# Optimization experiments

Hardware: AMD Instinct MI355X
Metric: run time of the kernel (lower is better)

Reference implementation:

```python
import jax, jax.numpy as jnp
import numpy as np

N_NODES = 100000
N_EDGES = 1600000
HIDDEN = 128
STEPS = 4
N_GRAPHS = 64


def setup_inputs() -> dict:
    key = jax.random.key(0)
    ks = jax.random.split(key, 8)
    x = jax.random.normal(ks[0], (N_NODES, HIDDEN), dtype=jnp.float32)
    edge_index = jax.random.randint(ks[1], (2, N_EDGES), 0, N_NODES, dtype=jnp.int64)
    batch = jnp.sort(jax.random.randint(ks[2], (N_NODES,), 0, N_GRAPHS, dtype=jnp.int64))
    s = 1.0 / np.sqrt(HIDDEN)
    weight = jax.random.normal(ks[3], (STEPS, HIDDEN, HIDDEN), dtype=jnp.float32) * s
    w_ih = jax.random.normal(ks[4], (3 * HIDDEN, HIDDEN), dtype=jnp.float32) * s
    w_hh = jax.random.normal(ks[5], (3 * HIDDEN, HIDDEN), dtype=jnp.float32) * s
    b_ih = jnp.zeros((3 * HIDDEN,), dtype=jnp.float32)
    b_hh = jnp.zeros((3 * HIDDEN,), dtype=jnp.float32)
    return {"x": x, "edge_index": edge_index, "batch": batch,
            "weight": weight, "w_ih": w_ih, "w_hh": w_hh,
            "b_ih": b_ih, "b_hh": b_hh}


def _gru_cell(m, h, w_ih, w_hh, b_ih, b_hh):
    # PyTorch GRUCell: gates ordered (r, z, n)
    gi = m @ w_ih.T + b_ih  # [N, 3H]
    gh = h @ w_hh.T + b_hh  # [N, 3H]
    i_r, i_z, i_n = jnp.split(gi, 3, axis=-1)
    h_r, h_z, h_n = jnp.split(gh, 3, axis=-1)
    r = jax.nn.sigmoid(i_r + h_r)
    z = jax.nn.sigmoid(i_z + h_z)
    n = jnp.tanh(i_n + r * h_n)
    return (1.0 - z) * n + z * h


def reference(x, edge_index, batch, weight, w_ih, w_hh, b_ih, b_hh):
    src, dst = edge_index[0], edge_index[1]
    h = x
    for i in range(STEPS):
        m = h @ weight[i]  # [N, H]
        # message = m[src] scattered (add) into dst
        aggr = jax.ops.segment_sum(m[src], dst, num_segments=N_NODES)
        h = _gru_cell(aggr, h, w_ih, w_hh, b_ih, b_hh)
    h = jax.nn.relu(h)
    # global mean pool per graph
    sums = jax.ops.segment_sum(h, batch, num_segments=N_GRAPHS)  # [G, H]
    counts = jax.ops.segment_sum(jnp.ones((N_NODES,), h.dtype), batch, num_segments=N_GRAPHS)
    return sums / jnp.maximum(counts, 1.0)[:, None]
```

## Files before the change

kernel.cpp:

```cpp
#include <hip/hip_runtime.h>

#define N_NODES  100000
#define N_EDGES  1600000
#define HIDDEN   128
#define STEPS    4
#define N_GRAPHS 64
#define NBUCK    256
#define BWID     391
#define BCAP     7168
#define OUT_P    136

typedef unsigned short u16;
typedef unsigned int   u32;
typedef unsigned long long u64;
typedef __attribute__((ext_vector_type(8))) short bf16x8;
typedef __attribute__((ext_vector_type(4))) float f32x4;

__device__ inline u16 f2bf(float f) {
  u32 u = __float_as_uint(f);
  u = (u + 0x7FFFu + ((u >> 16) & 1u)) >> 16;
  return (u16)u;
}
__device__ inline float bf2f(u16 b) { return __uint_as_float(((u32)b) << 16); }

__device__ inline float fast_sig(float x) { return 1.f / (1.f + __expf(-x)); }
__device__ inline float fast_tanh(float x) {
  x = fminf(fmaxf(x, -15.f), 15.f);
  float e = __expf(2.f * x);
  return (e - 1.f) / (e + 1.f);
}

__global__ __launch_bounds__(1024) void k_part(const int* __restrict__ esrc,
                                               const int* __restrict__ edst,
                                               int* __restrict__ gcursor,
                                               u64* __restrict__ ebuf) {
  __shared__ int hist[NBUCK];
  __shared__ int base[NBUCK];
  int tid = threadIdx.x;
  if (tid < NBUCK) hist[tid] = 0;
  __syncthreads();
  int e0 = blockIdx.x * 4096;
  int sv[4], dv[4], bk[4], rk[4];
  #pragma unroll
  for (int i = 0; i < 4; ++i) {
    int e = e0 + i * 1024 + tid;
    if (e < N_EDGES) {
      sv[i] = esrc[e];
      dv[i] = edst[e];
      bk[i] = (int)((u32)dv[i] / (u32)BWID);
      rk[i] = atomicAdd(&hist[bk[i]], 1);
    } else bk[i] = -1;
  }
  __syncthreads();
  if (tid < NBUCK) base[tid] = atomicAdd(&gcursor[tid], hist[tid]);
  __syncthreads();
  #pragma unroll
  for (int i = 0; i < 4; ++i) {
    if (bk[i] >= 0) {
      int pos = bk[i] * BCAP + base[bk[i]] + rk[i];
      ebuf[pos] = ((u64)(u32)dv[i] << 32) | (u32)sv[i];
    }
  }
}

__global__ void k_bscan(const int* __restrict__ gcursor, int* __restrict__ ebase) {
  __shared__ int buf[NBUCK];
  int t = threadIdx.x;
  int v = gcursor[t];
  buf[t] = v;
  __syncthreads();
  for (int off = 1; off < NBUCK; off <<= 1) {
    int u = 0;
    if (t >= off) u = buf[t - off];
    __syncthreads();
    buf[t] += u;
    __syncthreads();
  }
  ebase[t] = buf[t] - v;
  if (t == NBUCK - 1) ebase[NBUCK] = buf[t];
}

__global__ __launch_bounds__(1024) void k_csr(const u64* __restrict__ ebuf,
                                              const int* __restrict__ ebase,
                                              int* __restrict__ offs,
                                              int* __restrict__ csr) {
  __shared__ int lcnt[512];
  __shared__ int lofs[512];
  int b = blockIdx.x, tid = threadIdx.x;
  int n0 = b * BWID;
  int n1 = min(n0 + BWID, N_NODES);
  int nn = n1 - n0;
  int e0 = ebase[b];
  int cnt = ebase[b + 1] - e0;
  const u64* ebase_p = ebuf + (size_t)b * BCAP;
  if (tid < 512) lcnt[tid] = 0;
  __syncthreads();
  for (int e = tid; e < cnt; e += 1024) {
    int dst = (int)(ebase_p[e] >> 32);
    atomicAdd(&lcnt[dst - n0], 1);
  }
  __syncthreads();
  if (tid < 512) lofs[tid] = lcnt[tid];
  __syncthreads();
  for (int off = 1; off < 512; off <<= 1) {
    int v = 0;
    if (tid < 512 && tid >= off) v = lofs[tid - off];
    __syncthreads();
    if (tid < 512 && tid >= off) lofs[tid] += v;
    __syncthreads();
  }
  int nodeoff = 0;
  if (tid < 512) nodeoff = e0 + lofs[tid] - lcnt[tid];
  if (tid < 512) lofs[tid] = nodeoff;
  if (tid < nn) offs[n0 + tid] = nodeoff;
  if (b == 0 && tid == 0) offs[N_NODES] = N_EDGES;
  __syncthreads();
  for (int e = tid; e < cnt; e += 1024) {
    u64 p = ebase_p[e];
    int src = (int)(p & 0xffffffffull);
    int dst = (int)(p >> 32);
    int pos = atomicAdd(&lofs[dst - n0], 1);
    csr[pos] = src;
  }
}

__global__ void k_wb(const float* __restrict__ W, const float* __restrict__ w_ih,
                     const float* __restrict__ w_hh, u16* __restrict__ bsw) {
  __shared__ float wrow[128];
  int b = blockIdx.x, st = b >> 8, k = b & 255, t = threadIdx.x;
  if (k < 128) wrow[t] = W[(st * 128 + k) * 128 + t];
  __syncthreads();
  int kc = k >> 5, quad = (k >> 3) & 3, kl = k & 7;
  u16* base = bsw + (size_t)st * 131072 + kc * 16384;
  #pragma unroll
  for (int gq = 0; gq < 4; ++gq) {
    int c = gq * 128 + t;
    float v;
    if (k < 128) {
      if (c < 384) {
        const float* wr = w_ih + c * 128;
        float sacc = 0.f;
        for (int j = 0; j < 128; ++j) sacc += wrow[j] * wr[j];
        v = sacc;
      } else v = 0.f;
    } else {
      int kk = k - 128;
      if (c < 256)      v = w_hh[c * 128 + kk];
      else if (c < 384) v = 0.f;
      else              v = w_hh[(c - 128) * 128 + kk];
    }
    int gi = c >> 7, cw = c & 127;
    int wv = cw >> 5, hu = (cw >> 4) & 1, nl = c & 15;
    int slot = wv * 8 + gi * 2 + hu;
    base[(slot * 4 + quad) * 128 + nl * 8 + kl] = f2bf(v);
  }
}

__global__ void k_convert(const float* __restrict__ x, u16* __restrict__ h) {
  int i = (blockIdx.x * 256 + threadIdx.x) * 4;
  float4 v = *(const float4*)(x + i);
  u16 o[4] = {f2bf(v.x), f2bf(v.y), f2bf(v.z), f2bf(v.w)};
  *(uint2*)(h + i) = *(uint2*)o;
}

__global__ void k_gather(const u16* __restrict__ h, const int* __restrict__ csr,
                         const int* __restrict__ offs, u16* __restrict__ s) {
  int node = blockIdx.x * 4 + (threadIdx.x >> 6);
  int lane = threadIdx.x & 63;
  int beg = offs[node], end = offs[node + 1];
  float a0 = 0.f, a1 = 0.f;
  int j = beg;
  for (; j + 8 <= end; j += 8) {
    int i0 = csr[j],     i1 = csr[j + 1], i2 = csr[j + 2], i3 = csr[j + 3];
    int i4 = csr[j + 4], i5 = csr[j + 5], i6 = csr[j + 6], i7 = csr[j + 7];
    u32 v0 = *(const u32*)(h + (size_t)i0 * 128 + lane * 2);
    u32 v1 = *(const u32*)(h + (size_t)i1 * 128 + lane * 2);
    u32 v2 = *(const u32*)(h + (size_t)i2 * 128 + lane * 2);
    u32 v3 = *(const u32*)(h + (size_t)i3 * 128 + lane * 2);
    u32 v4 = *(const u32*)(h + (size_t)i4 * 128 + lane * 2);
    u32 v5 = *(const u32*)(h + (size_t)i5 * 128 + lane * 2);
    u32 v6 = *(const u32*)(h + (size_t)i6 * 128 + lane * 2);
    u32 v7 = *(const u32*)(h + (size_t)i7 * 128 + lane * 2);
    a0 += __uint_as_float(v0 << 16); a1 += __uint_as_float(v0 & 0xffff0000u);
    a0 += __uint_as_float(v1 << 16); a1 += __uint_as_float(v1 & 0xffff0000u);
    a0 += __uint_as_float(v2 << 16); a1 += __uint_as_float(v2 & 0xffff0000u);
    a0 += __uint_as_float(v3 << 16); a1 += __uint_as_float(v3 & 0xffff0000u);
    a0 += __uint_as_float(v4 << 16); a1 += __uint_as_float(v4 & 0xffff0000u);
    a0 += __uint_as_float(v5 << 16); a1 += __uint_as_float(v5 & 0xffff0000u);
    a0 += __uint_as_float(v6 << 16); a1 += __uint_as_float(v6 & 0xffff0000u);
    a0 += __uint_as_float(v7 << 16); a1 += __uint_as_float(v7 & 0xffff0000u);
  }
  for (; j < end; ++j) {
    int i0 = csr[j];
    u32 v0 = *(const u32*)(h + (size_t)i0 * 128 + lane * 2);
    a0 += __uint_as_float(v0 << 16);
    a1 += __uint_as_float(v0 & 0xffff0000u);
  }
  u32 o = (u32)f2bf(a0) | ((u32)f2bf(a1) << 16);
  *(u32*)(s + (size_t)node * 128 + lane * 2) = o;
}

__global__ __launch_bounds__(256, 3) void k_gemm_gru(
    const u16* __restrict__ s_mat, const u16* __restrict__ h_mat,
    const u16* __restrict__ bsw, const float* __restrict__ b_ih,
    const float* __restrict__ b_hh, u16* __restrict__ h_out) {
  __shared__ u16 Asw[8192];
  __shared__ u16 Osw[32 * OUT_P];

  const int tid  = threadIdx.x;
  const int wave = tid >> 6;
  const int lane = tid & 63;
  const int nl   = lane & 15;
  const int quad = lane >> 4;
  const int row0 = blockIdx.x * 32;

  {
    int snl = tid & 15, squad = (tid >> 4) & 3, sel = tid >> 6;
    int g = sel & 1, half = sel >> 1;
    const u16* row = (half ? h_mat : s_mat) + (size_t)(row0 + g * 16 + snl) * 128;
    #pragma unroll
    for (int kc2 = 0; kc2 < 4; ++kc2) {
      uint4 v = *(const uint4*)(row + kc2 * 32 + squad * 8);
      *(uint4*)&Asw[(((g * 8 + half * 4 + kc2) * 4 + squad) * 16 + snl) * 8] = v;
    }
  }
  __syncthreads();

  const u16* bp = bsw + wave * 8 * 512 + lane * 8;

  f32x4 acc[2][8];
  #pragma unroll
  for (int g = 0; g < 2; ++g)
    #pragma unroll
    for (int u = 0; u < 8; ++u) acc[g][u] = (f32x4){0.f, 0.f, 0.f, 0.f};

  bf16x8 bcur[6], bnext[6];
  #pragma unroll
  for (int i = 0; i < 6; ++i) bcur[i] = *(const bf16x8*)(bp + i * 512);

  #pragma unroll
  for (int kc = 0; kc < 8; ++kc) {
    if (kc < 7) {
      #pragma unroll
      for (int i = 0; i < 6; ++i) {
        int us = (kc + 1 < 4) ? i : (i < 4 ? i : i + 2);
        bnext[i] = *(const bf16x8*)(bp + (kc + 1) * 16384 + us * 512);
      }
    }
    bf16x8 a0 = *(const bf16x8*)&Asw[kc * 512 + lane * 8];
    bf16x8 a1 = *(const bf16x8*)&Asw[(8 + kc) * 512 + lane * 8];
    #pragma unroll
    for (int i = 0; i < 6; ++i) {
      int u = (kc < 4) ? i : (i < 4 ? i : i + 2);
      acc[0][u] = __builtin_amdgcn_mfma_f32_16x16x32_bf16(a0, bcur[i], acc[0][u], 0, 0, 0);
      acc[1][u] = __builtin_amdgcn_mfma_f32_16x16x32_bf16(a1, bcur[i], acc[1][u], 0, 0, 0);
    }
    #pragma unroll
    for (int i = 0; i < 6; ++i) bcur[i] = bnext[i];
  }

  float bias[8];
  #pragma unroll
  for (int u = 0; u < 8; ++u) {
    int gi = u >> 1, hu = u & 1;
    int cw = wave * 32 + hu * 16 + nl;
    bias[u] = (gi == 0) ? b_ih[cw] + b_hh[cw]
            : (gi == 1) ? b_ih[128 + cw] + b_hh[128 + cw]
            : (gi == 2) ? b_ih[256 + cw]
                        : b_hh[256 + cw];
  }

  #pragma unroll
  for (int g = 0; g < 2; ++g) {
    #pragma unroll
    for (int hu = 0; hu < 2; ++hu) {
      int cw = wave * 32 + hu * 16 + nl;
      int hbase = ((g * 8 + 4 + wave) * 4 + ((hu * 2 + (nl >> 3)) & 3)) * 128 + (nl & 7);
      #pragma unroll
      for (int i = 0; i < 4; ++i) {
        int m = quad * 4 + i;
        float rv = fast_sig(acc[g][0 + hu][i] + bias[0 + hu]);
        float zv = fast_sig(acc[g][2 + hu][i] + bias[2 + hu]);
        float iv = acc[g][4 + hu][i] + bias[4 + hu];
        float hn = acc[g][6 + hu][i] + bias[6 + hu];
        float hv = bf2f(Asw[hbase + m * 8]);
        float n  = fast_tanh(iv + rv * hn);
        float o  = (1.f - zv) * n + zv * hv;
        Osw[(g * 16 + m) * OUT_P + cw] = f2bf(o);
      }
    }
  }
  __syncthreads();

  {
    int r32 = tid >> 3, c0 = (tid & 7) * 16;
    uint4 v0 = *(const uint4*)&Osw[r32 * OUT_P + c0];
    uint4 v1 = *(const uint4*)&Osw[r32 * OUT_P + c0 + 8];
    uint4* dstp = (uint4*)(h_out + (size_t)(row0 + r32) * 128 + c0);
    dstp[0] = v0;
    dstp[1] = v1;
  }
}

__global__ void k_pool_partial(const u16* __restrict__ h, const int* __restrict__ batch,
                               float* __restrict__ acc) {
  int t = threadIdx.x;
  int node0 = blockIdx.x * 125;
  int node1 = node0 + 125;
  int cur = batch[node0];
  float sum = 0.f;
  for (int r = node0; r < node1; ++r) {
    int g = batch[r];
    if (g != cur) {
      atomicAdd(&acc[cur * 128 + t], sum);
      sum = 0.f;
      cur = g;
    }
    sum += fmaxf(bf2f(h[(size_t)r * 128 + t]), 0.f);
  }
  atomicAdd(&acc[cur * 128 + t], sum);
}

__global__ void k_pool_div(const float* __restrict__ acc, const int* __restrict__ batch,
                           float* __restrict__ out) {
  __shared__ int se[2];
  int g = blockIdx.x, t = threadIdx.x;
  if (t < 2) {
    int target = g + t;
    int lo = 0, hi = N_NODES;
    while (lo < hi) { int mid = (lo + hi) >> 1; if (batch[mid] < target) lo = mid + 1; else hi = mid; }
    se[t] = lo;
  }
  __syncthreads();
  int cnt = se[1] - se[0];
  out[g * 128 + t] = acc[g * 128 + t] / (float)(cnt > 0 ? cnt : 1);
}

extern "C" void kernel_launch(void* const* d_in, const int* in_sizes, int n_in,
                              void* d_out, int out_size, void* d_ws, size_t ws_size,
                              hipStream_t stream) {
  const float* x     = (const float*)d_in[0];
  const int*   edges = (const int*)d_in[1];
  const int*   batch = (const int*)d_in[2];
  const float* W     = (const float*)d_in[3];
  const float* w_ih  = (const float*)d_in[4];
  const float* w_hh  = (const float*)d_in[5];
  const float* b_ih  = (const float*)d_in[6];
  const float* b_hh  = (const float*)d_in[7];
  float* out = (float*)d_out;

  char* w = (char*)d_ws;
  u16* buf0    = (u16*)(w);
  u16* buf1    = (u16*)(w + 25600000);
  u16* bsw     = (u16*)(w + 51200000);
  float* acc   = (float*)(w + 52300032);
  int* offs    = (int*)(w + 52710400);
  int* gcursor = (int*)(w + 53120768);
  int* ebase   = (int*)(w + 53123328);
  int* csr     = (int*)(w + 53531136);
  u64* ebuf    = (u64*)buf1;

  const int* esrc = edges;
  const int* edst = edges + N_EDGES;

  hipMemsetAsync(gcursor, 0, NBUCK * sizeof(int), stream);
  k_part<<<391, 1024, 0, stream>>>(esrc, edst, gcursor, ebuf);
  k_bscan<<<1, NBUCK, 0, stream>>>(gcursor, ebase);
  k_csr<<<NBUCK, 1024, 0, stream>>>(ebuf, ebase, offs, csr);
  k_wb<<<1024, 128, 0, stream>>>(W, w_ih, w_hh, bsw);
  k_convert<<<(N_NODES * HIDDEN) / 1024, 256, 0, stream>>>(x, buf0);
  hipMemsetAsync(acc, 0, N_GRAPHS * HIDDEN * sizeof(float), stream);

  u16* hcur = buf0;
  u16* hnxt = buf1;
  for (int st = 0; st < STEPS; ++st) {
    k_gather<<<N_NODES / 4, 256, 0, stream>>>(hcur, csr, offs, hnxt);
    k_gemm_gru<<<N_NODES / 32, 256, 0, stream>>>(hnxt, hcur, bsw + st * 131072,
                                                 b_ih, b_hh, hnxt);
    u16* tmp = hcur; hcur = hnxt; hnxt = tmp;
  }
  k_pool_partial<<<800, 128, 0, stream>>>(hcur, batch, acc);
  k_pool_div<<<N_GRAPHS, 128, 0, stream>>>(acc, batch, out);
}
```

Before: 674.8 us.

## Fuse neighbor gather into GEMM+GRU kernel, writing aggregates straight to LDS

Merges the separate gather kernel into the per-step GEMM/GRU kernel. Each block now sums the neighbor rows for its 32 nodes, using 16-byte loads spread over four edge streams and reduced with shuffles, and writes the bf16 aggregates directly into the swizzled shared-memory A tile. This removes one launch per step and the global write and reread of the aggregate matrix. In exchange, gather parallelism is tied to the GEMM grid and launch bounds, with waves handling 8 nodes serially, which can lower latency hiding for the random loads.

```diff
diff --git a/kernel.cpp b/kernel.cpp
--- a/kernel.cpp
+++ b/kernel.cpp
@@ -163,47 +163,18 @@
   *(uint2*)(h + i) = *(uint2*)o;
 }
 
-__global__ void k_gather(const u16* __restrict__ h, const int* __restrict__ csr,
-                         const int* __restrict__ offs, u16* __restrict__ s) {
-  int node = blockIdx.x * 4 + (threadIdx.x >> 6);
-  int lane = threadIdx.x & 63;
-  int beg = offs[node], end = offs[node + 1];
-  float a0 = 0.f, a1 = 0.f;
-  int j = beg;
-  for (; j + 8 <= end; j += 8) {
-    int i0 = csr[j],     i1 = csr[j + 1], i2 = csr[j + 2], i3 = csr[j + 3];
-    int i4 = csr[j + 4], i5 = csr[j + 5], i6 = csr[j + 6], i7 = csr[j + 7];
-    u32 v0 = *(const u32*)(h + (size_t)i0 * 128 + lane * 2);
-    u32 v1 = *(const u32*)(h + (size_t)i1 * 128 + lane * 2);
-    u32 v2 = *(const u32*)(h + (size_t)i2 * 128 + lane * 2);
-    u32 v3 = *(const u32*)(h + (size_t)i3 * 128 + lane * 2);
-    u32 v4 = *(const u32*)(h + (size_t)i4 * 128 + lane * 2);
-    u32 v5 = *(const u32*)(h + (size_t)i5 * 128 + lane * 2);
-    u32 v6 = *(const u32*)(h + (size_t)i6 * 128 + lane * 2);
-    u32 v7 = *(const u32*)(h + (size_t)i7 * 128 + lane * 2);
-    a0 += __uint_as_float(v0 << 16); a1 += __uint_as_float(v0 & 0xffff0000u);
-    a0 += __uint_as_float(v1 << 16); a1 += __uint_as_float(v1 & 0xffff0000u);
-    a0 += __uint_as_float(v2 << 16); a1 += __uint_as_float(v2 & 0xffff0000u);
-    a0 += __uint_as_float(v3 << 16); a1 += __uint_as_float(v3 & 0xffff0000u);
-    a0 += __uint_as_float(v4 << 16); a1 += __uint_as_float(v4 & 0xffff0000u);
-    a0 += __uint_as_float(v5 << 16); a1 += __uint_as_float(v5 & 0xffff0000u);
-    a0 += __uint_as_float(v6 << 16); a1 += __uint_as_float(v6 & 0xffff0000u);
-    a0 += __uint_as_float(v7 << 16); a1 += __uint_as_float(v7 & 0xffff0000u);
-  }
-  for (; j < end; ++j) {
-    int i0 = csr[j];
-    u32 v0 = *(const u32*)(h + (size_t)i0 * 128 + lane * 2);
-    a0 += __uint_as_float(v0 << 16);
-    a1 += __uint_as_float(v0 & 0xffff0000u);
-  }
-  u32 o = (u32)f2bf(a0) | ((u32)f2bf(a1) << 16);
-  *(u32*)(s + (size_t)node * 128 + lane * 2) = o;
-}
-
-__global__ __launch_bounds__(256, 3) void k_gemm_gru(
-    const u16* __restrict__ s_mat, const u16* __restrict__ h_mat,
-    const u16* __restrict__ bsw, const float* __restrict__ b_ih,
-    const float* __restrict__ b_hh, u16* __restrict__ h_out) {
+__device__ inline void acc8(float* a, uint4 p) {
+  a[0] += bf2f((u16)(p.x & 0xffffu)); a[1] += bf2f((u16)(p.x >> 16));
+  a[2] += bf2f((u16)(p.y & 0xffffu)); a[3] += bf2f((u16)(p.y >> 16));
+  a[4] += bf2f((u16)(p.z & 0xffffu)); a[5] += bf2f((u16)(p.z >> 16));
+  a[6] += bf2f((u16)(p.w & 0xffffu)); a[7] += bf2f((u16)(p.w >> 16));
+}
+
+__global__ __launch_bounds__(256, 3) void k_mpnn_step(
+    const u16* __restrict__ h_mat, const int* __restrict__ csr,
+    const int* __restrict__ offs, const u16* __restrict__ bsw,
+    const float* __restrict__ b_ih, const float* __restrict__ b_hh,
+    u16* __restrict__ h_out) {
   __shared__ u16 Asw[8192];
   __shared__ u16 Osw[32 * OUT_P];
 
@@ -215,13 +186,53 @@
   const int row0 = blockIdx.x * 32;
 
   {
-    int snl = tid & 15, squad = (tid >> 4) & 3, sel = tid >> 6;
-    int g = sel & 1, half = sel >> 1;
-    const u16* row = (half ? h_mat : s_mat) + (size_t)(row0 + g * 16 + snl) * 128;
-    #pragma unroll
-    for (int kc2 = 0; kc2 < 4; ++kc2) {
-      uint4 v = *(const uint4*)(row + kc2 * 32 + squad * 8);
-      *(uint4*)&Asw[(((g * 8 + half * 4 + kc2) * 4 + squad) * 16 + snl) * 8] = v;
+    int r = tid >> 3;
+    int g = r >> 4, snl = r & 15;
+    const u16* row = h_mat + (size_t)(row0 + r) * 128;
+    #pragma unroll
+    for (int t2 = 0; t2 < 2; ++t2) {
+      int cb = (tid & 7) * 2 + t2;
+      int kc2 = cb >> 2, squad = cb & 3;
+      uint4 v = *(const uint4*)(row + cb * 8);
+      *(uint4*)&Asw[(((g * 8 + 4 + kc2) * 4 + squad) * 16 + snl) * 8] = v;
+    }
+  }
+
+  {
+    int q = quad, sub = nl;
+    for (int i = 0; i < 8; ++i) {
+      int nloc = wave * 8 + i;
+      int node = row0 + nloc;
+      int beg = offs[node], end = offs[node + 1];
+      float a[8] = {0.f, 0.f, 0.f, 0.f, 0.f, 0.f, 0.f, 0.f};
+      int j = beg + q;
+      for (; j + 12 < end; j += 16) {
+        int s0 = csr[j], s1 = csr[j + 4], s2 = csr[j + 8], s3 = csr[j + 12];
+        uint4 p0 = *(const uint4*)(h_mat + (size_t)s0 * 128 + sub * 8);
+        uint4 p1 = *(const uint4*)(h_mat + (size_t)s1 * 128 + sub * 8);
+        uint4 p2 = *(const uint4*)(h_mat + (size_t)s2 * 128 + sub * 8);
+        uint4 p3 = *(const uint4*)(h_mat + (size_t)s3 * 128 + sub * 8);
+        acc8(a, p0); acc8(a, p1); acc8(a, p2); acc8(a, p3);
+      }
+      for (; j < end; j += 4) {
+        uint4 p0 = *(const uint4*)(h_mat + (size_t)csr[j] * 128 + sub * 8);
+        acc8(a, p0);
+      }
+      #pragma unroll
+      for (int v = 0; v < 8; ++v) {
+        a[v] += __shfl_xor(a[v], 16);
+        a[v] += __shfl_xor(a[v], 32);
+      }
+      if (q == 0) {
+        int g = nloc >> 4, snl = nloc & 15;
+        int kc2 = sub >> 2, squad = sub & 3;
+        uint4 o;
+        o.x = (u32)f2bf(a[0]) | ((u32)f2bf(a[1]) << 16);
+        o.y = (u32)f2bf(a[2]) | ((u32)f2bf(a[3]) << 16);
+        o.z = (u32)f2bf(a[4]) | ((u32)f2bf(a[5]) << 16);
+        o.w = (u32)f2bf(a[6]) | ((u32)f2bf(a[7]) << 16);
+        *(uint4*)&Asw[(((g * 8 + kc2) * 4 + squad) * 16 + snl) * 8] = o;
+      }
     }
   }
   __syncthreads();
@@ -374,9 +385,9 @@
   u16* hcur = buf0;
   u16* hnxt = buf1;
   for (int st = 0; st < STEPS; ++st) {
-    k_gather<<<N_NODES / 4, 256, 0, stream>>>(hcur, csr, offs, hnxt);
-    k_gemm_gru<<<N_NODES / 32, 256, 0, stream>>>(hnxt, hcur, bsw + st * 131072,
-                                                 b_ih, b_hh, hnxt);
+    k_mpnn_step<<<N_NODES / 32, 256, 0, stream>>>(hcur, csr, offs,
+                                                  bsw + st * 131072,
+                                                  b_ih, b_hh, hnxt);
     u16* tmp = hcur; hcur = hnxt; hnxt = tmp;
   }
   k_pool_partial<<<800, 128, 0, stream>>>(hcur, batch, acc);
```

Result: slower. 771.7 us (+14.4%).
